# Optimization experiments

Hardware: AMD Instinct MI355X
Metric: run time of the kernel (lower is better)

The kernel has to match this reference:

```python
import jax, jax.numpy as jnp
import numpy as np
from jax import lax


def _conv(x, w, padding):
    # NCHW input, OIHW weights, stride 1, no bias
    return lax.conv_general_dilated(x, w, (1, 1), padding,
                                    dimension_numbers=('NCHW', 'OIHW', 'NCHW'))


def setup_inputs() -> dict:
    key = jax.random.key(0)
    ks = jax.random.split(key, 6)
    B, C, H, W = 16, 512, 40, 40
    return {
        'exemplar': jax.random.normal(ks[0], (B, C, H, W), jnp.float32),
        'query':    jax.random.normal(ks[1], (B, C, H, W), jnp.float32),
        'w_e':  jax.random.normal(ks[2], (256, C, 1, 1), jnp.float32) * 0.01,
        'w_q':  jax.random.normal(ks[3], (256, C, 1, 1), jnp.float32) * 0.01,
        'w_c1': jax.random.normal(ks[4], (C, C, 3, 3), jnp.float32) * 0.01,
        'w_c2': jax.random.normal(ks[5], (C, C, 3, 3), jnp.float32) * 0.01,
    }


def reference(exemplar, query, w_e, w_q, w_c1, w_c2):
    B, C, H, W = query.shape
    N = H * W
    # 1x1 projections to 256-dim correlation space
    q_corr = _conv(query, w_q, 'VALID').reshape(B, -1, N)     # [B,256,N]
    e_corr = _conv(exemplar, w_e, 'VALID').reshape(B, -1, N)  # [B,256,N]
    # A[b, n_exemplar, m_query] = <e_corr[:, n], q_corr[:, m]>
    A = jnp.einsum('bcn,bcm->bnm', e_corr, q_corr)            # [B,N,N]
    # A1 = softmax over exemplar axis, then transpose (torch: softmax(A,dim=1).T)
    A1 = jnp.swapaxes(jax.nn.softmax(A, axis=1), 1, 2)        # [B,N,N]
    # Bm = softmax(A^T, dim=1).T  == softmax(A, axis=2)
    Bm = jnp.swapaxes(jax.nn.softmax(jnp.swapaxes(A, 1, 2), axis=1), 1, 2)
    e_flat = exemplar.reshape(B, C, N)
    q_flat = query.reshape(B, C, N)
    query_att = jnp.matmul(e_flat, A1)   # [B,C,N]
    exemplar_att = jnp.matmul(q_flat, Bm)  # [B,C,N]
    input1_att = _conv(exemplar_att.reshape(B, C, H, W), w_c1, 'SAME')
    input2_att = _conv(query_att.reshape(B, C, H, W), w_c2, 'SAME')
    return jnp.concatenate([input1_att, input2_att], axis=1)  # [B,2C,H,W]
```

## Files before the change

### kernel.cpp

```cpp
#include <hip/hip_runtime.h>

typedef unsigned short u16;
typedef __attribute__((ext_vector_type(8))) short bf16x8;
typedef __attribute__((ext_vector_type(4))) float f32x4;

__device__ __forceinline__ u16 f2bf(float f) {
  union { float f; unsigned u; } v; v.f = f;
  unsigned u = v.u;
  u += 0x7fffu + ((u >> 16) & 1u);
  return (u16)(u >> 16);
}

__device__ __forceinline__ void gll16(const void* g, void* l) {
  __builtin_amdgcn_global_load_lds(
      (const __attribute__((address_space(1))) void*)g,
      (__attribute__((address_space(3))) void*)l, 16, 0, 0);
}

__global__ __launch_bounds__(256) void transp_cast_x2(const float* __restrict__ ex,
                                                      const float* __restrict__ qu,
                                                      u16* __restrict__ xte,
                                                      u16* __restrict__ xtq) {
  __shared__ float t[32][33];
  int z = blockIdx.z;
  int b = z & 15;
  const float* xb = (z < 16 ? ex : qu) + (size_t)b * 819200;
  u16* xtb = (z < 16 ? xte : xtq) + (size_t)b * 819200;
  int n0 = blockIdx.x * 32, c0 = blockIdx.y * 32;
  int tx = threadIdx.x & 31, ty = threadIdx.x >> 5;
#pragma unroll
  for (int k = 0; k < 4; k++) {
    int c = ty + k * 8;
    t[c][tx] = xb[(size_t)(c0 + c) * 1600 + n0 + tx];
  }
  __syncthreads();
#pragma unroll
  for (int k = 0; k < 4; k++) {
    int n = ty + k * 8;
    xtb[(size_t)(n0 + n) * 512 + c0 + tx] = f2bf(t[tx][n]);
  }
}

__global__ void cast_w(const float* __restrict__ we, const float* __restrict__ wq,
                       u16* __restrict__ oe, u16* __restrict__ oq) {
  int i = blockIdx.x * 256 + threadIdx.x;
  oe[i] = f2bf(we[i]);
  oq[i] = f2bf(wq[i]);
}

__global__ void repack_wc(const float* __restrict__ w1, const float* __restrict__ w2,
                          u16* __restrict__ o1, u16* __restrict__ o2) {
  const float* w = blockIdx.y ? w2 : w1;
  u16* wr = blockIdx.y ? o2 : o1;
  int idx = blockIdx.x * 256 + threadIdx.x;
  int o = idx / 4608;
  int r = idx - o * 4608;
  int t = r >> 9;
  int c = r & 511;
  wr[idx] = f2bf(w[o * 4608 + c * 9 + t]);
}

__global__ void zero_mem(uint4* __restrict__ p, long n) {
  long i = (long)blockIdx.x * blockDim.x + threadIdx.x;
  long stride = (long)gridDim.x * blockDim.x;
  uint4 z; z.x = 0; z.y = 0; z.z = 0; z.w = 0;
  for (; i < n; i += stride) p[i] = z;
}

template <int MODE>
__global__ __launch_bounds__(256) void gemm_bt64(
    const u16* __restrict__ A, const u16* __restrict__ B, u16* __restrict__ C,
    const u16* __restrict__ A2, const u16* __restrict__ B2, u16* __restrict__ C2,
    int M, int N, int K, long sA, long sB, long sC) {
  __shared__ u16 lds_a[128 * 64];
  __shared__ u16 lds_b[128 * 64];
  int tid = threadIdx.x;
  int z = blockIdx.z, b = z & 15;
  const u16* Ab = (z < 16 ? A : A2) + (size_t)b * sA;
  const u16* Bb = (z < 16 ? B : B2) + (size_t)b * sB;
  u16* Cb = (z < 16 ? C : C2) + (size_t)b * sC;
  int m0 = blockIdx.x * 128, n0 = blockIdx.y * 128;

  int rsub = tid >> 3;
  int gch = (tid & 7) ^ (rsub & 7);
  long Kb = (long)K * 2;
  const char* pa[4];
  const char* pb[4];
#pragma unroll
  for (int c = 0; c < 4; c++) {
    int ra = m0 + 32 * c + rsub; ra = ra < M ? ra : M - 1;
    int rb = n0 + 32 * c + rsub; rb = rb < N ? rb : N - 1;
    pa[c] = (const char*)Ab + (long)ra * Kb + gch * 16;
    pb[c] = (const char*)Bb + (long)rb * Kb + gch * 16;
  }

  const f32x4 fzero = {0.f, 0.f, 0.f, 0.f};
  f32x4 acc[4][4];
#pragma unroll
  for (int mi = 0; mi < 4; mi++)
#pragma unroll
    for (int ni = 0; ni < 4; ni++) acc[mi][ni] = fzero;

  int wid = tid >> 6, lane = tid & 63;
  int wm = wid & 1, wn = wid >> 1;
  int lrow = lane & 15, lquad = lane >> 4;
  int sl = lrow & 7;

  int ksteps = K >> 6;
  for (int ks = 0; ks < ksteps; ks++) {
#pragma unroll
    for (int c = 0; c < 4; c++) {
      gll16(pa[c], (char*)lds_a + c * 4096 + tid * 16);
      gll16(pb[c], (char*)lds_b + c * 4096 + tid * 16);
      pa[c] += 128; pb[c] += 128;
    }
    __syncthreads();
#pragma unroll
    for (int k2 = 0; k2 < 2; k2++) {
      int sel = ((k2 << 2) | lquad) ^ sl;
      bf16x8 bv[4];
#pragma unroll
      for (int ni = 0; ni < 4; ni++) {
        int rowb = wn * 64 + ni * 16 + lrow;
        bv[ni] = *(const bf16x8*)((const char*)lds_b + rowb * 128 + sel * 16);
      }
#pragma unroll
      for (int mi = 0; mi < 4; mi++) {
        int rowa = wm * 64 + mi * 16 + lrow;
        bf16x8 av = *(const bf16x8*)((const char*)lds_a + rowa * 128 + sel * 16);
#pragma unroll
        for (int ni = 0; ni < 4; ni++)
          acc[mi][ni] =
              __builtin_amdgcn_mfma_f32_16x16x32_bf16(av, bv[ni], acc[mi][ni], 0, 0, 0);
      }
    }
    __syncthreads();
  }

#pragma unroll
  for (int mi = 0; mi < 4; mi++) {
#pragma unroll
    for (int r = 0; r < 4; r++) {
      int i = m0 + wm * 64 + mi * 16 + lquad * 4 + r;
      if (i >= M) continue;
#pragma unroll
      for (int ni = 0; ni < 4; ni++) {
        int j = n0 + wn * 64 + ni * 16 + lrow;
        if (j >= N) continue;
        float v = acc[mi][ni][r];
        if (MODE == 2) {
          int y = i / 40, x = i - y * 40;
          Cb[(size_t)((y + 1) * 42 + (x + 1)) * 512 + j] = f2bf(v);
        } else {
          Cb[(size_t)i * N + j] = f2bf(v);
        }
      }
    }
  }
}

__global__ __launch_bounds__(256) void gemm_corr_exp(
    const u16* __restrict__ A, const u16* __restrict__ B, u16* __restrict__ E,
    u16* __restrict__ ET, float* __restrict__ Zrow, float* __restrict__ Zcol) {
  __shared__ u16 lds_a[128 * 64];
  __shared__ u16 lds_b[128 * 64];
  int tid = threadIdx.x;
  int b = blockIdx.z;
  const u16* Ab = A + (size_t)b * 409600;
  const u16* Bb = B + (size_t)b * 409600;
  u16* Eb = E + (size_t)b * 2560000;
  u16* ETb = ET + (size_t)b * 2560000;
  int m0 = blockIdx.x * 128, n0 = blockIdx.y * 128;

  int rsub = tid >> 3;
  int gch = (tid & 7) ^ (rsub & 7);
  const char* pa[4];
  const char* pb[4];
#pragma unroll
  for (int c = 0; c < 4; c++) {
    int ra = m0 + 32 * c + rsub; ra = ra < 1600 ? ra : 1599;
    int rb = n0 + 32 * c + rsub; rb = rb < 1600 ? rb : 1599;
    pa[c] = (const char*)(Ab + (size_t)ra * 256) + gch * 16;
    pb[c] = (const char*)(Bb + (size_t)rb * 256) + gch * 16;
  }

  const f32x4 fzero = {0.f, 0.f, 0.f, 0.f};
  f32x4 acc[4][4];
#pragma unroll
  for (int mi = 0; mi < 4; mi++)
#pragma unroll
    for (int ni = 0; ni < 4; ni++) acc[mi][ni] = fzero;

  int wid = tid >> 6, lane = tid & 63;
  int wm = wid & 1, wn = wid >> 1;
  int lrow = lane & 15, lquad = lane >> 4;
  int sl = lrow & 7;

  for (int ks = 0; ks < 4; ks++) {
#pragma unroll
    for (int c = 0; c < 4; c++) {
      gll16(pa[c], (char*)lds_a + c * 4096 + tid * 16);
      gll16(pb[c], (char*)lds_b + c * 4096 + tid * 16);
      pa[c] += 128; pb[c] += 128;
    }
    __syncthreads();
#pragma unroll
    for (int k2 = 0; k2 < 2; k2++) {
      int sel = ((k2 << 2) | lquad) ^ sl;
      bf16x8 bv[4];
#pragma unroll
      for (int ni = 0; ni < 4; ni++) {
        int rowb = wn * 64 + ni * 16 + lrow;
        bv[ni] = *(const bf16x8*)((const char*)lds_b + rowb * 128 + sel * 16);
      }
#pragma unroll
      for (int mi = 0; mi < 4; mi++) {
        int rowa = wm * 64 + mi * 16 + lrow;
        bf16x8 av = *(const bf16x8*)((const char*)lds_a + rowa * 128 + sel * 16);
#pragma unroll
        for (int ni = 0; ni < 4; ni++)
          acc[mi][ni] =
              __builtin_amdgcn_mfma_f32_16x16x32_bf16(av, bv[ni], acc[mi][ni], 0, 0, 0);
      }
    }
    __syncthreads();
  }

  const int TS = 136;
  u16* T = lds_a;
  float colacc[4] = {0.f, 0.f, 0.f, 0.f};
#pragma unroll
  for (int s = 0; s < 4; s++) {
    if (wm == (s >> 1)) {
      int smi0 = (s & 1) * 2;
#pragma unroll
      for (int mi2 = 0; mi2 < 2; mi2++) {
        int mi = smi0 + mi2;
        float rowp[4] = {0.f, 0.f, 0.f, 0.f};
#pragma unroll
        for (int ni = 0; ni < 4; ni++) {
          int j = n0 + wn * 64 + ni * 16 + lrow;
          bool jv = j < 1600;
#pragma unroll
          for (int r = 0; r < 4; r++) {
            int i = m0 + wm * 64 + mi * 16 + lquad * 4 + r;
            float e = __expf(acc[mi][ni][r]);
            T[(mi2 * 16 + lquad * 4 + r) * TS + wn * 64 + ni * 16 + lrow] = f2bf(e);
            rowp[r] += jv ? e : 0.f;
            colacc[ni] += (i < 1600) ? e : 0.f;
          }
        }
#pragma unroll
        for (int r = 0; r < 4; r++) {
          float v = rowp[r];
          v += __shfl_xor(v, 1);
          v += __shfl_xor(v, 2);
          v += __shfl_xor(v, 4);
          v += __shfl_xor(v, 8);
          int i = m0 + wm * 64 + mi * 16 + lquad * 4 + r;
          if (lrow == 0 && i < 1600) atomicAdd(&Zrow[b * 1600 + i], v);
        }
      }
    }
    __syncthreads();
#pragma unroll
    for (int p = 0; p < 2; p++) {
      int jj = tid + p * 256;
      int ml = jj >> 4, n8 = jj & 15;
      int gi = m0 + s * 32 + ml, gj = n0 + n8 * 8;
      if (gi < 1600 && gj < 1600)
        *(uint4*)(Eb + (size_t)gi * 1600 + gj) = *(const uint4*)&T[ml * TS + n8 * 8];
    }
#pragma unroll
    for (int p = 0; p < 4; p++) {
      int jj = tid + p * 256;
      int n = jj >> 3, m4 = jj & 7;
      int gm = m0 + s * 32 + m4 * 4, gn = n0 + n;
      if (gn < 1600 && gm < 1600) {
        ushort4 v;
        v.x = T[(m4 * 4 + 0) * TS + n];
        v.y = T[(m4 * 4 + 1) * TS + n];
        v.z = T[(m4 * 4 + 2) * TS + n];
        v.w = T[(m4 * 4 + 3) * TS + n];
        *(ushort4*)(ETb + (size_t)gn * 1600 + gm) = v;
      }
    }
    __syncthreads();
  }
#pragma unroll
  for (int ni = 0; ni < 4; ni++) {
    float v = colacc[ni];
    v += __shfl_xor(v, 16);
    v += __shfl_xor(v, 32);
    int j = n0 + wn * 64 + ni * 16 + lrow;
    if (lquad == 0 && j < 1600) atomicAdd(&Zcol[b * 1600 + j], v);
  }
}

__global__ void scale_div(const float* __restrict__ ex, const float* __restrict__ qu,
                          const float* __restrict__ Zcol, const float* __restrict__ Zrow,
                          u16* __restrict__ ebf, u16* __restrict__ qbf) {
  const float* x; const float* Z; u16* o;
  if (blockIdx.y == 0) { x = ex; Z = Zcol; o = ebf; }
  else { x = qu; Z = Zrow; o = qbf; }
  size_t idx = (size_t)blockIdx.x * 256 + threadIdx.x;
  int b = (int)(idx / 819200);
  int i = (int)(idx % 1600);
  o[idx] = f2bf(x[idx] / Z[b * 1600 + i]);
}

__global__ __launch_bounds__(512, 2) void conv_gemmpf(
    const u16* __restrict__ W1, const u16* __restrict__ ATT1,
    const u16* __restrict__ W2, const u16* __restrict__ ATT2,
    float* __restrict__ out) {
  __shared__ u16 ldsA[32768];
  __shared__ u16 ldsB[32768];
  int tid = threadIdx.x;
  int z = blockIdx.z, b = z & 15, sel2 = z >> 4;
  const u16* W = sel2 ? W2 : W1;
  const u16* attb = (sel2 ? ATT2 : ATT1) + (size_t)b * 903168;
  float* outb = out + (size_t)b * 1638400 + (size_t)(sel2 ? 512 : 0) * 1600;
  int p0 = blockIdx.x * 224, o0 = blockIdx.y * 256;

  int rl = tid >> 2;
  int cs = (tid & 3) ^ ((rl >> 1) & 3);
  const char* pA0 = (const char*)(W + (size_t)(o0 + rl) * 4608) + cs * 16;
  const char* pA1 = pA0 + 128 * 9216;
  int pp0 = p0 + rl; pp0 = pp0 < 1600 ? pp0 : 1599;
  int y0 = pp0 / 40, x0 = pp0 - y0 * 40;
  const char* pB0 = (const char*)(attb + (size_t)(y0 * 42 + x0) * 512) + cs * 16;
  int pp1 = p0 + 128 + rl; pp1 = pp1 < 1600 ? pp1 : 1599;
  int y1 = pp1 / 40, x1 = pp1 - y1 * 40;
  const char* pB1 = (const char*)(attb + (size_t)(y1 * 42 + x1) * 512) + cs * 16;

  char* ldsAb = (char*)ldsA;
  char* ldsBb = (char*)ldsB;
  int dstT = tid * 16;

#define STAGE_A(d, kh, kt)                                              \
  {                                                                     \
    int ko = (kt) * 128 + (kh) * 64;                                    \
    gll16(pA0 + ko, ldsAb + ((d) * 2 + (kh)) * 16384 + dstT);           \
    gll16(pA1 + ko, ldsAb + ((d) * 2 + (kh)) * 16384 + 8192 + dstT);    \
  }
#define STAGE_B(d, kh, kt)                                              \
  {                                                                     \
    int tp = (kt) >> 3;                                                 \
    int ty = (tp * 11) >> 5;                                            \
    int tx = tp - ty * 3;                                               \
    int ko = (ty * 42 + tx) * 1024 + ((kt) & 7) * 128 + (kh) * 64;      \
    gll16(pB0 + ko, ldsBb + ((d) * 2 + (kh)) * 16384 + dstT);           \
    gll16(pB1 + ko, ldsBb + ((d) * 2 + (kh)) * 16384 + 8192 + dstT);    \
  }
#define STAGE_U(d, kh, kt) { STAGE_A(d, kh, kt); STAGE_B(d, kh, kt); }

  int wid = tid >> 6, lane = tid & 63;
  int wm = wid & 3, wn = wid >> 2;
  int lrow = lane & 15, lquad = lane >> 4;
  int csel = (lquad ^ ((lrow >> 1) & 3)) << 4;
  int aBase = (wm * 64 + lrow) * 64 + csel;
  int bBase = (wn * 112 + lrow) * 64 + csel;

  const f32x4 fzero = {0.f, 0.f, 0.f, 0.f};
  f32x4 acc[4][7];
#pragma unroll
  for (int mi = 0; mi < 4; mi++)
#pragma unroll
    for (int ni = 0; ni < 7; ni++) acc[mi][ni] = fzero;

  bf16x8 fa0, fa1, fa2, fa3, fb0, fb1, fb2, fb3, fb4, fb5, fb6;
  bf16x8 ga0, ga1, ga2, ga3, gb0, gb1, gb2, gb3, gb4, gb5, gb6;

#define RD(pre, d, kh)                                                  \
  {                                                                     \
    const char* ra_ = ldsAb + ((d) * 2 + (kh)) * 16384 + aBase;         \
    const char* rb_ = ldsBb + ((d) * 2 + (kh)) * 16384 + bBase;         \
    pre##a0 = *(const bf16x8*)(ra_);                                    \
    pre##a1 = *(const bf16x8*)(ra_ + 1024);                             \
    pre##a2 = *(const bf16x8*)(ra_ + 2048);                             \
    pre##a3 = *(const bf16x8*)(ra_ + 3072);                             \
    pre##b0 = *(const bf16x8*)(rb_);                                    \
    pre##b1 = *(const bf16x8*)(rb_ + 1024);                             \
    pre##b2 = *(const bf16x8*)(rb_ + 2048);                             \
    pre##b3 = *(const bf16x8*)(rb_ + 3072);                             \
    pre##b4 = *(const bf16x8*)(rb_ + 4096);                             \
    pre##b5 = *(const bf16x8*)(rb_ + 5120);                             \
    pre##b6 = *(const bf16x8*)(rb_ + 6144);                             \
  }

#define MROW(mi, av, pre)                                                               \
  acc[mi][0] = __builtin_amdgcn_mfma_f32_16x16x32_bf16(av, pre##b0, acc[mi][0], 0, 0, 0); \
  acc[mi][1] = __builtin_amdgcn_mfma_f32_16x16x32_bf16(av, pre##b1, acc[mi][1], 0, 0, 0); \
  acc[mi][2] = __builtin_amdgcn_mfma_f32_16x16x32_bf16(av, pre##b2, acc[mi][2], 0, 0, 0); \
  acc[mi][3] = __builtin_amdgcn_mfma_f32_16x16x32_bf16(av, pre##b3, acc[mi][3], 0, 0, 0); \
  acc[mi][4] = __builtin_amdgcn_mfma_f32_16x16x32_bf16(av, pre##b4, acc[mi][4], 0, 0, 0); \
  acc[mi][5] = __builtin_amdgcn_mfma_f32_16x16x32_bf16(av, pre##b5, acc[mi][5], 0, 0, 0); \
  acc[mi][6] = __builtin_amdgcn_mfma_f32_16x16x32_bf16(av, pre##b6, acc[mi][6], 0, 0, 0);

#define PHASE(rd_d, rd_kh, rdp, cp, STG)                                       \
  {                                                                            \
    STG;                                                                       \
    asm volatile("s_waitcnt vmcnt(4)" ::: "memory");                           \
    __builtin_amdgcn_s_barrier();                                              \
    RD(rdp, rd_d, rd_kh);                                                      \
    __builtin_amdgcn_s_setprio(1);                                             \
    MROW(0, cp##a0, cp)                                                        \
    MROW(1, cp##a1, cp)                                                        \
    MROW(2, cp##a2, cp)                                                        \
    MROW(3, cp##a3, cp)                                                        \
    __builtin_amdgcn_s_setprio(0);                                             \
  }

  STAGE_U(0, 0, 0);
  STAGE_U(0, 1, 0);
  asm volatile("s_waitcnt vmcnt(4)" ::: "memory");
  __builtin_amdgcn_s_barrier();
  RD(f, 0, 0);

#pragma unroll 1
  for (int it = 0; it < 36; ++it) {
    int kt1 = it * 2 + 1;
    int kt2 = it < 35 ? it * 2 + 2 : 71;
    PHASE(0, 1, g, f, STAGE_U(1, 0, kt1));
    PHASE(1, 0, f, g, STAGE_U(1, 1, kt1));
    PHASE(1, 1, g, f, STAGE_U(0, 0, kt2));
    PHASE(0, 0, f, g, STAGE_U(0, 1, kt2));
  }

#undef PHASE
#undef MROW
#undef RD
#undef STAGE_U
#undef STAGE_A
#undef STAGE_B

#pragma unroll
  for (int mi = 0; mi < 4; mi++) {
#pragma unroll
    for (int r = 0; r < 4; r++) {
      int o = o0 + wm * 64 + mi * 16 + lquad * 4 + r;
      float* orow = outb + (size_t)o * 1600;
#pragma unroll
      for (int ni = 0; ni < 7; ni++) {
        int p = p0 + wn * 112 + ni * 16 + lrow;
        if (p < 1600) orow[p] = acc[mi][ni][r];
      }
    }
  }
}

extern "C" void kernel_launch(void* const* d_in, const int* in_sizes, int n_in,
                              void* d_out, int out_size, void* d_ws, size_t ws_size,
                              hipStream_t stream) {
  const float* ex = (const float*)d_in[0];
  const float* qu = (const float*)d_in[1];
  const float* w_e = (const float*)d_in[2];
  const float* w_q = (const float*)d_in[3];
  const float* w_c1 = (const float*)d_in[4];
  const float* w_c2 = (const float*)d_in[5];
  float* out = (float*)d_out;
  char* ws = (char*)d_ws;

  u16* E     = (u16*)(ws + 0L);
  u16* ET    = (u16*)(ws + 81920000L);
  u16* xt_e  = (u16*)(ws + 163840000L);
  u16* xt_q  = (u16*)(ws + 190054400L);
  u16* ecorr = (u16*)(ws + 216268800L);
  u16* qcorr = (u16*)(ws + 229376000L);
  u16* att_e = (u16*)(ws + 242483200L);
  u16* att_q = (u16*)(ws + 271384576L);
  float* Zrow = (float*)(ws + 300285952L);
  float* Zcol = (float*)(ws + 300388352L);
  u16* w_ebf = (u16*)(ws + 300490752L);
  u16* w_qbf = (u16*)(ws + 300752896L);
  u16* wr1   = (u16*)(ws + 301015040L);
  u16* wr2   = (u16*)(ws + 305733632L);

  transp_cast_x2<<<dim3(50, 16, 32), 256, 0, stream>>>(ex, qu, xt_e, xt_q);
  cast_w<<<dim3(512), 256, 0, stream>>>(w_e, w_q, w_ebf, w_qbf);
  repack_wc<<<dim3(9216, 2), 256, 0, stream>>>(w_c1, w_c2, wr1, wr2);
  zero_mem<<<dim3(2048), 256, 0, stream>>>((uint4*)att_e, 3625472L);

  gemm_bt64<0><<<dim3(13, 2, 32), 256, 0, stream>>>(
      xt_e, w_ebf, ecorr, xt_q, w_qbf, qcorr, 1600, 256, 512, 819200L, 0L, 409600L);

  gemm_corr_exp<<<dim3(13, 13, 16), 256, 0, stream>>>(ecorr, qcorr, E, ET, Zrow, Zcol);

  u16* ebf = xt_e;
  u16* qbf = xt_q;
  scale_div<<<dim3(51200, 2), 256, 0, stream>>>(ex, qu, Zcol, Zrow, ebf, qbf);

  gemm_bt64<2><<<dim3(13, 4, 32), 256, 0, stream>>>(
      E, ebf, att_q, ET, qbf, att_e, 1600, 512, 1600, 2560000L, 819200L, 903168L);

  conv_gemmpf<<<dim3(8, 2, 32), 512, 0, stream>>>(wr1, att_e, wr2, att_q, out);
}
```

Baseline: 831.0 us.

## Replace attention-apply GEMM with larger-tile pipelined kernel and XCD-aware block remap

The attention-apply GEMM (softmax weights times features) moves off the generic 128x128 gemm_bt64 kernel onto a new 512-thread kernel. It reuses the conv kernel's 256x224 tile, its double-buffered direct-to-LDS load pipeline, and its prioritized MFMA schedule over K=1600. Blocks are remapped so consecutive work items are spread across chiplets. The epilogue writes into the padded NHWC layout that the conv kernel expects, which dropped MODE 2 from the old GEMM. The goal is higher MFMA utilization and better operand reuse, at the cost of fewer, larger blocks and more register pressure.

```diff
diff --git a/kernel.cpp b/kernel.cpp
--- a/kernel.cpp
+++ b/kernel.cpp
@@ -147,13 +147,7 @@
       for (int ni = 0; ni < 4; ni++) {
         int j = n0 + wn * 64 + ni * 16 + lrow;
         if (j >= N) continue;
-        float v = acc[mi][ni][r];
-        if (MODE == 2) {
-          int y = i / 40, x = i - y * 40;
-          Cb[(size_t)((y + 1) * 42 + (x + 1)) * 512 + j] = f2bf(v);
-        } else {
-          Cb[(size_t)i * N + j] = f2bf(v);
-        }
+        Cb[(size_t)i * N + j] = f2bf(acc[mi][ni][r]);
       }
     }
   }
@@ -309,50 +303,43 @@
   o[idx] = f2bf(x[idx] / Z[b * 1600 + i]);
 }
 
-__global__ __launch_bounds__(512, 2) void conv_gemmpf(
-    const u16* __restrict__ W1, const u16* __restrict__ ATT1,
-    const u16* __restrict__ W2, const u16* __restrict__ ATT2,
-    float* __restrict__ out) {
+__global__ __launch_bounds__(512, 2) void att_gemmpf(
+    const u16* __restrict__ Aw1, const u16* __restrict__ Bp1, u16* __restrict__ C1,
+    const u16* __restrict__ Aw2, const u16* __restrict__ Bp2, u16* __restrict__ C2) {
   __shared__ u16 ldsA[32768];
   __shared__ u16 ldsB[32768];
   int tid = threadIdx.x;
-  int z = blockIdx.z, b = z & 15, sel2 = z >> 4;
-  const u16* W = sel2 ? W2 : W1;
-  const u16* attb = (sel2 ? ATT2 : ATT1) + (size_t)b * 903168;
-  float* outb = out + (size_t)b * 1638400 + (size_t)(sel2 ? 512 : 0) * 1600;
-  int p0 = blockIdx.x * 224, o0 = blockIdx.y * 256;
+  int flat = blockIdx.x + (blockIdx.y << 3) + (blockIdx.z << 4);
+  int wrk = (flat & 7) * 64 + (flat >> 3);
+  int z = wrk >> 4, rr = wrk & 15;
+  int bx = rr & 7, by = rr >> 3;
+  int b = z & 15;
+  const u16* Aw = (z < 16 ? Aw1 : Aw2) + (size_t)b * 819200;
+  const u16* Bp = (z < 16 ? Bp1 : Bp2) + (size_t)b * 2560000;
+  u16* Cb = (z < 16 ? C1 : C2) + (size_t)b * 903168;
+  int p0 = bx * 224, o0 = by * 256;
 
   int rl = tid >> 2;
   int cs = (tid & 3) ^ ((rl >> 1) & 3);
-  const char* pA0 = (const char*)(W + (size_t)(o0 + rl) * 4608) + cs * 16;
-  const char* pA1 = pA0 + 128 * 9216;
+  const char* pA0 = (const char*)(Aw + (size_t)(o0 + rl) * 1600) + cs * 16;
+  const char* pA1 = pA0 + 128 * 3200;
   int pp0 = p0 + rl; pp0 = pp0 < 1600 ? pp0 : 1599;
-  int y0 = pp0 / 40, x0 = pp0 - y0 * 40;
-  const char* pB0 = (const char*)(attb + (size_t)(y0 * 42 + x0) * 512) + cs * 16;
+  const char* pB0 = (const char*)(Bp + (size_t)pp0 * 1600) + cs * 16;
   int pp1 = p0 + 128 + rl; pp1 = pp1 < 1600 ? pp1 : 1599;
-  int y1 = pp1 / 40, x1 = pp1 - y1 * 40;
-  const char* pB1 = (const char*)(attb + (size_t)(y1 * 42 + x1) * 512) + cs * 16;
+  const char* pB1 = (const char*)(Bp + (size_t)pp1 * 1600) + cs * 16;
 
   char* ldsAb = (char*)ldsA;
   char* ldsBb = (char*)ldsB;
   int dstT = tid * 16;
 
-#define STAGE_A(d, kh, kt)                                              \
+#define STAGE_U(d, kh, kt)                                              \
   {                                                                     \
     int ko = (kt) * 128 + (kh) * 64;                                    \
     gll16(pA0 + ko, ldsAb + ((d) * 2 + (kh)) * 16384 + dstT);           \
     gll16(pA1 + ko, ldsAb + ((d) * 2 + (kh)) * 16384 + 8192 + dstT);    \
-  }
-#define STAGE_B(d, kh, kt)                                              \
-  {                                                                     \
-    int tp = (kt) >> 3;                                                 \
-    int ty = (tp * 11) >> 5;                                            \
-    int tx = tp - ty * 3;                                               \
-    int ko = (ty * 42 + tx) * 1024 + ((kt) & 7) * 128 + (kh) * 64;      \
     gll16(pB0 + ko, ldsBb + ((d) * 2 + (kh)) * 16384 + dstT);           \
     gll16(pB1 + ko, ldsBb + ((d) * 2 + (kh)) * 16384 + 8192 + dstT);    \
   }
-#define STAGE_U(d, kh, kt) { STAGE_A(d, kh, kt); STAGE_B(d, kh, kt); }
 
   int wid = tid >> 6, lane = tid & 63;
   int wm = wid & 3, wn = wid >> 2;
@@ -418,6 +405,153 @@
   RD(f, 0, 0);
 
 #pragma unroll 1
+  for (int it = 0; it < 12; ++it) {
+    int kt1 = it * 2 + 1;
+    int kt2 = it * 2 + 2;
+    PHASE(0, 1, g, f, STAGE_U(1, 0, kt1));
+    PHASE(1, 0, f, g, STAGE_U(1, 1, kt1));
+    PHASE(1, 1, g, f, STAGE_U(0, 0, kt2));
+    PHASE(0, 0, f, g, STAGE_U(0, 1, kt2));
+  }
+  asm volatile("s_waitcnt vmcnt(0)" ::: "memory");
+  __builtin_amdgcn_s_barrier();
+  RD(g, 0, 1);
+  __builtin_amdgcn_s_setprio(1);
+  MROW(0, fa0, f) MROW(1, fa1, f) MROW(2, fa2, f) MROW(3, fa3, f)
+  MROW(0, ga0, g) MROW(1, ga1, g) MROW(2, ga2, g) MROW(3, ga3, g)
+  __builtin_amdgcn_s_setprio(0);
+
+#undef PHASE
+#undef MROW
+#undef RD
+#undef STAGE_U
+
+#pragma unroll
+  for (int mi = 0; mi < 4; mi++) {
+#pragma unroll
+    for (int r = 0; r < 4; r++) {
+      int o = o0 + wm * 64 + mi * 16 + lquad * 4 + r;
+#pragma unroll
+      for (int ni = 0; ni < 7; ni++) {
+        int p = p0 + wn * 112 + ni * 16 + lrow;
+        if (p < 1600) {
+          int y = p / 40, x = p - y * 40;
+          Cb[(size_t)((y + 1) * 42 + (x + 1)) * 512 + o] = f2bf(acc[mi][ni][r]);
+        }
+      }
+    }
+  }
+}
+
+__global__ __launch_bounds__(512, 2) void conv_gemmpf(
+    const u16* __restrict__ W1, const u16* __restrict__ ATT1,
+    const u16* __restrict__ W2, const u16* __restrict__ ATT2,
+    float* __restrict__ out) {
+  __shared__ u16 ldsA[32768];
+  __shared__ u16 ldsB[32768];
+  int tid = threadIdx.x;
+  int z = blockIdx.z, b = z & 15, sel2 = z >> 4;
+  const u16* W = sel2 ? W2 : W1;
+  const u16* attb = (sel2 ? ATT2 : ATT1) + (size_t)b * 903168;
+  float* outb = out + (size_t)b * 1638400 + (size_t)(sel2 ? 512 : 0) * 1600;
+  int p0 = blockIdx.x * 224, o0 = blockIdx.y * 256;
+
+  int rl = tid >> 2;
+  int cs = (tid & 3) ^ ((rl >> 1) & 3);
+  const char* pA0 = (const char*)(W + (size_t)(o0 + rl) * 4608) + cs * 16;
+  const char* pA1 = pA0 + 128 * 9216;
+  int pp0 = p0 + rl; pp0 = pp0 < 1600 ? pp0 : 1599;
+  int y0 = pp0 / 40, x0 = pp0 - y0 * 40;
+  const char* pB0 = (const char*)(attb + (size_t)(y0 * 42 + x0) * 512) + cs * 16;
+  int pp1 = p0 + 128 + rl; pp1 = pp1 < 1600 ? pp1 : 1599;
+  int y1 = pp1 / 40, x1 = pp1 - y1 * 40;
+  const char* pB1 = (const char*)(attb + (size_t)(y1 * 42 + x1) * 512) + cs * 16;
+
+  char* ldsAb = (char*)ldsA;
+  char* ldsBb = (char*)ldsB;
+  int dstT = tid * 16;
+
+#define STAGE_A(d, kh, kt)                                              \
+  {                                                                     \
+    int ko = (kt) * 128 + (kh) * 64;                                    \
+    gll16(pA0 + ko, ldsAb + ((d) * 2 + (kh)) * 16384 + dstT);           \
+    gll16(pA1 + ko, ldsAb + ((d) * 2 + (kh)) * 16384 + 8192 + dstT);    \
+  }
+#define STAGE_B(d, kh, kt)                                              \
+  {                                                                     \
+    int tp = (kt) >> 3;                                                 \
+    int ty = (tp * 11) >> 5;                                            \
+    int tx = tp - ty * 3;                                               \
+    int ko = (ty * 42 + tx) * 1024 + ((kt) & 7) * 128 + (kh) * 64;      \
+    gll16(pB0 + ko, ldsBb + ((d) * 2 + (kh)) * 16384 + dstT);           \
+    gll16(pB1 + ko, ldsBb + ((d) * 2 + (kh)) * 16384 + 8192 + dstT);    \
+  }
+#define STAGE_U(d, kh, kt) { STAGE_A(d, kh, kt); STAGE_B(d, kh, kt); }
+
+  int wid = tid >> 6, lane = tid & 63;
+  int wm = wid & 3, wn = wid >> 2;
+  int lrow = lane & 15, lquad = lane >> 4;
+  int csel = (lquad ^ ((lrow >> 1) & 3)) << 4;
+  int aBase = (wm * 64 + lrow) * 64 + csel;
+  int bBase = (wn * 112 + lrow) * 64 + csel;
+
+  const f32x4 fzero = {0.f, 0.f, 0.f, 0.f};
+  f32x4 acc[4][7];
+#pragma unroll
+  for (int mi = 0; mi < 4; mi++)
+#pragma unroll
+    for (int ni = 0; ni < 7; ni++) acc[mi][ni] = fzero;
+
+  bf16x8 fa0, fa1, fa2, fa3, fb0, fb1, fb2, fb3, fb4, fb5, fb6;
+  bf16x8 ga0, ga1, ga2, ga3, gb0, gb1, gb2, gb3, gb4, gb5, gb6;
+
+#define RD(pre, d, kh)                                                  \
+  {                                                                     \
+    const char* ra_ = ldsAb + ((d) * 2 + (kh)) * 16384 + aBase;         \
+    const char* rb_ = ldsBb + ((d) * 2 + (kh)) * 16384 + bBase;         \
+    pre##a0 = *(const bf16x8*)(ra_);                                    \
+    pre##a1 = *(const bf16x8*)(ra_ + 1024);                             \
+    pre##a2 = *(const bf16x8*)(ra_ + 2048);                             \
+    pre##a3 = *(const bf16x8*)(ra_ + 3072);                             \
+    pre##b0 = *(const bf16x8*)(rb_);                                    \
+    pre##b1 = *(const bf16x8*)(rb_ + 1024);                             \
+    pre##b2 = *(const bf16x8*)(rb_ + 2048);                             \
+    pre##b3 = *(const bf16x8*)(rb_ + 3072);                             \
+    pre##b4 = *(const bf16x8*)(rb_ + 4096);                             \
+    pre##b5 = *(const bf16x8*)(rb_ + 5120);                             \
+    pre##b6 = *(const bf16x8*)(rb_ + 6144);                             \
+  }
+
+#define MROW(mi, av, pre)                                                               \
+  acc[mi][0] = __builtin_amdgcn_mfma_f32_16x16x32_bf16(av, pre##b0, acc[mi][0], 0, 0, 0); \
+  acc[mi][1] = __builtin_amdgcn_mfma_f32_16x16x32_bf16(av, pre##b1, acc[mi][1], 0, 0, 0); \
+  acc[mi][2] = __builtin_amdgcn_mfma_f32_16x16x32_bf16(av, pre##b2, acc[mi][2], 0, 0, 0); \
+  acc[mi][3] = __builtin_amdgcn_mfma_f32_16x16x32_bf16(av, pre##b3, acc[mi][3], 0, 0, 0); \
+  acc[mi][4] = __builtin_amdgcn_mfma_f32_16x16x32_bf16(av, pre##b4, acc[mi][4], 0, 0, 0); \
+  acc[mi][5] = __builtin_amdgcn_mfma_f32_16x16x32_bf16(av, pre##b5, acc[mi][5], 0, 0, 0); \
+  acc[mi][6] = __builtin_amdgcn_mfma_f32_16x16x32_bf16(av, pre##b6, acc[mi][6], 0, 0, 0);
+
+#define PHASE(rd_d, rd_kh, rdp, cp, STG)                                       \
+  {                                                                            \
+    STG;                                                                       \
+    asm volatile("s_waitcnt vmcnt(4)" ::: "memory");                           \
+    __builtin_amdgcn_s_barrier();                                              \
+    RD(rdp, rd_d, rd_kh);                                                      \
+    __builtin_amdgcn_s_setprio(1);                                             \
+    MROW(0, cp##a0, cp)                                                        \
+    MROW(1, cp##a1, cp)                                                        \
+    MROW(2, cp##a2, cp)                                                        \
+    MROW(3, cp##a3, cp)                                                        \
+    __builtin_amdgcn_s_setprio(0);                                             \
+  }
+
+  STAGE_U(0, 0, 0);
+  STAGE_U(0, 1, 0);
+  asm volatile("s_waitcnt vmcnt(4)" ::: "memory");
+  __builtin_amdgcn_s_barrier();
+  RD(f, 0, 0);
+
+#pragma unroll 1
   for (int it = 0; it < 36; ++it) {
     int kt1 = it * 2 + 1;
     int kt2 = it < 35 ? it * 2 + 2 : 71;
@@ -490,8 +624,7 @@
   u16* qbf = xt_q;
   scale_div<<<dim3(51200, 2), 256, 0, stream>>>(ex, qu, Zcol, Zrow, ebf, qbf);
 
-  gemm_bt64<2><<<dim3(13, 4, 32), 256, 0, stream>>>(
-      E, ebf, att_q, ET, qbf, att_e, 1600, 512, 1600, 2560000L, 819200L, 903168L);
+  att_gemmpf<<<dim3(8, 2, 32), 512, 0, stream>>>(ebf, E, att_q, qbf, ET, att_e);
 
   conv_gemmpf<<<dim3(8, 2, 32), 512, 0, stream>>>(wr1, att_e, wr2, att_q, out);
 }
```

Result: faster. 806.1 us (-3.0%).
